# Optimization experiments

Measured on AMD Instinct MI355X. Metric: run time of the kernel, lower is better.

The kernel has to match this reference:

```python
import jax, jax.numpy as jnp
import numpy as np
from jax.scipy.special import logsumexp

B, T, D, C = 64, 512, 1024, 32


def setup_inputs() -> dict:
    key = jax.random.key(0)
    ks = jax.random.split(key, 6)
    vectors = jax.random.normal(ks[0], (B, T, D), dtype=jnp.float32)
    mask = jnp.ones((B, T), dtype=jnp.int32)
    targets = jax.random.randint(ks[1], (B, T), 0, C)
    W = jax.random.normal(ks[2], (C, D), dtype=jnp.float32) * 0.02
    b = jnp.zeros((C,), dtype=jnp.float32)
    transitions = jax.random.normal(ks[3], (C, C), dtype=jnp.float32) * 0.1
    start_transitions = jax.random.normal(ks[4], (C,), dtype=jnp.float32) * 0.1
    end_transitions = jax.random.normal(ks[5], (C,), dtype=jnp.float32) * 0.1
    return {"vectors": vectors, "mask": mask, "targets": targets, "W": W, "b": b,
            "transitions": transitions, "start_transitions": start_transitions,
            "end_transitions": end_transitions}


def reference(vectors, mask, targets, W, b, transitions, start_transitions, end_transitions):
    n_classes = transitions.shape[0]
    # projection: [B,T,C]
    logits = jnp.einsum('btd,cd->btc', vectors, W) + b
    maskf = mask.astype(logits.dtype)

    # time-major views for scan
    logits_tm = jnp.swapaxes(logits, 0, 1)   # [T,B,C]
    mask_tm = jnp.swapaxes(maskf, 0, 1)      # [T,B]

    # ---- CRF partition function (forward algorithm, log-sum-exp recurrence) ----
    def fwd_step(alpha, xs):
        lt, mt = xs                                      # [B,C], [B]
        inner = alpha[:, :, None] + transitions[None] + lt[:, None, :]  # [B,C,C]
        new = logsumexp(inner, axis=1)                   # [B,C]
        alpha = jnp.where(mt[:, None] > 0, new, alpha)
        return alpha, None

    alpha0 = start_transitions[None, :] + logits_tm[0]
    alpha, _ = jax.lax.scan(fwd_step, alpha0, (logits_tm[1:], mask_tm[1:]))
    log_Z = logsumexp(alpha + end_transitions[None, :], axis=-1)  # [B]

    # ---- joint (numerator) score of the target path, AllenNLP semantics ----
    emit = jnp.take_along_axis(logits, targets[..., None], axis=-1)[..., 0]  # [B,T]
    trans_sc = transitions[targets[:, :-1], targets[:, 1:]]                  # [B,T-1]
    score = start_transitions[targets[:, 0]]
    score = score + jnp.sum(trans_sc * maskf[:, 1:], axis=1)
    score = score + jnp.sum(emit[:, :-1] * maskf[:, :-1], axis=1)
    last_idx = jnp.sum(mask, axis=1).astype(jnp.int32) - 1                   # [B]
    last_tags = jnp.take_along_axis(targets, last_idx[:, None], axis=1)[:, 0]
    score = score + end_transitions[last_tags]
    score = score + jnp.take_along_axis(logits[:, -1], last_tags[:, None], axis=1)[:, 0] * maskf[:, -1]

    # loss = -log_likelihood / num_tokens
    loss = -jnp.sum(score - log_Z) / jnp.sum(maskf)

    # ---- Viterbi decoding (max-product DP + backtrace) ----
    def vit_step(delta, xs):
        lt, mt = xs
        inner = delta[:, :, None] + transitions[None]    # [B,C,C] (prev x next)
        bp = jnp.argmax(inner, axis=1)                   # [B,C]
        best = jnp.max(inner, axis=1) + lt
        new_delta = jnp.where(mt[:, None] > 0, best, delta)
        bp = jnp.where(mt[:, None] > 0, bp, jnp.arange(n_classes)[None, :])
        return new_delta, bp

    delta0 = start_transitions[None, :] + logits_tm[0]
    delta, bps = jax.lax.scan(vit_step, delta0, (logits_tm[1:], mask_tm[1:]))  # bps [T-1,B,C]
    final = delta + end_transitions[None, :]
    path_scores = jnp.max(final, axis=-1)                # [B]
    last_tag = jnp.argmax(final, axis=-1)                # [B]

    def back_step(tag, bp_t):
        prev = jnp.take_along_axis(bp_t, tag[:, None], axis=1)[:, 0]
        return prev, tag

    first_tag, tags_rev = jax.lax.scan(back_step, last_tag, bps, reverse=True)  # ys[t] = tag at t+1
    tags = jnp.concatenate([first_tag[:, None], jnp.swapaxes(tags_rev, 0, 1)], axis=1)  # [B,T]

    return loss, logits, tags, path_scores
```

## Files before the change

kernel.cpp:

```cpp
#include <hip/hip_runtime.h>

#define B_ 64
#define T_ 512
#define D_ 1024
#define C_ 32
#define KCH 64
#define CHUNK 16
#define NCHUNK (T_ / CHUNK)
#define NEG_INF (-1e30f)

__device__ __forceinline__ float bcast0(float v) {
  return __uint_as_float(__builtin_amdgcn_readfirstlane(__float_as_uint(v)));
}
__device__ __forceinline__ float rlane(float v, int l) {
  return __uint_as_float(__builtin_amdgcn_readlane(__float_as_uint(v), l));
}

__global__ __launch_bounds__(256) void k_logits(const float* __restrict__ vec,
                                                const float* __restrict__ W,
                                                const float* __restrict__ bias,
                                                float* __restrict__ out) {
  __shared__ __align__(16) float vt[64][KCH + 4];
  __shared__ __align__(16) float wt[32][KCH + 4];
  const int tid = threadIdx.x;
  const int cg = tid & 7;
  const int rg = tid >> 3;
  const int r0 = blockIdx.x * 64;
  const int sr = tid >> 4;
  const int sq = tid & 15;
  const int wr = tid >> 3;
  const int wq = tid & 7;
  float acc[2][4];
#pragma unroll
  for (int a = 0; a < 2; ++a)
#pragma unroll
    for (int bb = 0; bb < 4; ++bb) acc[a][bb] = 0.f;

  for (int c = 0; c < D_ / KCH; ++c) {
    const int k0 = c * KCH;
    __syncthreads();
#pragma unroll
    for (int p = 0; p < 4; ++p) {
      const int r = p * 16 + sr;
      float4 v = *(const float4*)(vec + (size_t)(r0 + r) * D_ + k0 + sq * 4);
      *(float4*)&vt[r][sq * 4] = v;
    }
    {
      float4 a = *(const float4*)(W + (size_t)wr * D_ + k0 + wq * 4);
      float4 b2 = *(const float4*)(W + (size_t)wr * D_ + k0 + (wq + 8) * 4);
      *(float4*)&wt[wr][wq * 4] = a;
      *(float4*)&wt[wr][(wq + 8) * 4] = b2;
    }
    __syncthreads();
#pragma unroll 2
    for (int k = 0; k < KCH; k += 4) {
      float4 v[2], w[4];
#pragma unroll
      for (int rr = 0; rr < 2; ++rr) v[rr] = *(const float4*)&vt[rg + rr * 32][k];
#pragma unroll
      for (int cc = 0; cc < 4; ++cc) w[cc] = *(const float4*)&wt[cg + cc * 8][k];
#pragma unroll
      for (int rr = 0; rr < 2; ++rr)
#pragma unroll
        for (int cc = 0; cc < 4; ++cc) {
          acc[rr][cc] = fmaf(v[rr].x, w[cc].x, acc[rr][cc]);
          acc[rr][cc] = fmaf(v[rr].y, w[cc].y, acc[rr][cc]);
          acc[rr][cc] = fmaf(v[rr].z, w[cc].z, acc[rr][cc]);
          acc[rr][cc] = fmaf(v[rr].w, w[cc].w, acc[rr][cc]);
        }
    }
  }
#pragma unroll
  for (int rr = 0; rr < 2; ++rr) {
    const size_t row = (size_t)(r0 + rg + rr * 32);
#pragma unroll
    for (int cc = 0; cc < 4; ++cc) {
      const int c = cg + cc * 8;
      out[row * C_ + c] = acc[rr][cc] + bias[c];
    }
  }
}

__global__ __launch_bounds__(64) void k_crf(const float* __restrict__ lg,
                                            const int* __restrict__ mask,
                                            const int* __restrict__ tgt,
                                            const float* __restrict__ trans,
                                            const float* __restrict__ st,
                                            const float* __restrict__ et,
                                            float* __restrict__ wsp,
                                            float* __restrict__ tags_out,
                                            float* __restrict__ path_out) {
  __shared__ __align__(16) float dsh[256 * C_];
  __shared__ __align__(16) float a_sh[C_];
  __shared__ __align__(16) float Lsh[2][CHUNK * C_];
  __shared__ float s0_sh[T_];
  __shared__ int mk_sh[T_];
  __shared__ unsigned char bp[(T_ - 1) * C_];
  __shared__ unsigned char tagb[T_];
  __shared__ unsigned char c8[64 * C_];
  __shared__ int btag[64];

  const int tid = threadIdx.x;
  const int b = blockIdx.x & 63;
  const int role = blockIdx.x >> 6;
  const int j = tid & 31;
  const int h = tid >> 5;
  const float* L = lg + (size_t)b * T_ * C_;
  const int* mk = mask + b * T_;

  float pre[8];
#pragma unroll
  for (int i = 0; i < 8; ++i) pre[i] = L[i * 64 + tid];
  {
    int4 m0 = *(const int4*)(mk + tid * 4);
    int4 m1 = *(const int4*)(mk + 256 + tid * 4);
    *(int4*)&mk_sh[tid * 4] = m0;
    *(int4*)&mk_sh[256 + tid * 4] = m1;
  }

  if (role == 0) {
    float ET[32];
#pragma unroll
    for (int i = 0; i < 32; ++i) ET[i] = __expf(trans[i * C_ + j]);
    const float a0j = st[j] + L[j];
    const float m0 = bcast0(a0j);
    float vp = __expf(a0j - m0);
    a_sh[j] = vp;
#pragma unroll
    for (int i = 0; i < 8; ++i) {
      const float b0v = rlane(pre[i], 0);
      const float b1v = rlane(pre[i], 32);
      const float base = (tid < 32) ? b0v : b1v;
      Lsh[0][i * 64 + tid] = __expf(pre[i] - base);
    }
    for (int c = 0; c < NCHUNK; ++c) {
      if (c < NCHUNK - 1) {
#pragma unroll
        for (int i = 0; i < 8; ++i) pre[i] = L[(c + 1) * (CHUNK * C_) + i * 64 + tid];
      }
      const float* Fs = Lsh[c & 1];
      const int tlo = c ? c * CHUNK : 1;
      const int thi = c * CHUNK + CHUNK;
      for (int t = tlo; t < thi; ++t) {
        const float Fv = Fs[(t - c * CHUNK) * C_ + j];
        const int mc = mk_sh[t];
        float4 q = *(const float4*)&a_sh[0];
        float s0 = q.x * ET[0], s1 = q.y * ET[1], s2 = q.z * ET[2], s3 = q.w * ET[3];
#pragma unroll
        for (int g = 1; g < 8; ++g) {
          q = *(const float4*)&a_sh[g * 4];
          s0 = fmaf(q.x, ET[4 * g + 0], s0);
          s1 = fmaf(q.y, ET[4 * g + 1], s1);
          s2 = fmaf(q.z, ET[4 * g + 2], s2);
          s3 = fmaf(q.w, ET[4 * g + 3], s3);
        }
        const float sv = (s0 + s1) + (s2 + s3);
        const float s0b = bcast0(sv);
        const float r = __builtin_amdgcn_rcpf(s0b);
        const float pn = sv * r * Fv;
        vp = (mc > 0) ? pn : vp;
        if (tid == 0) s0_sh[t] = (mc > 0) ? s0b : 1.0f;
        a_sh[j] = vp;
      }
      if (c < NCHUNK - 1) {
#pragma unroll
        for (int i = 0; i < 8; ++i) {
          const float b0v = rlane(pre[i], 0);
          const float b1v = rlane(pre[i], 32);
          const float base = (tid < 32) ? b0v : b1v;
          Lsh[(c & 1) ^ 1][i * 64 + tid] = __expf(pre[i] - base);
        }
      }
    }
    float lsum = 0.f, csum = 0.f;
#pragma unroll
    for (int kk = 0; kk < 8; ++kk) {
      const int t = tid + kk * 64;
      if (t >= 1) {
        lsum += __logf(s0_sh[t]);
        if (mk_sh[t] > 0) csum += L[(size_t)t * C_];
      }
    }
#pragma unroll
    for (int d = 32; d; d >>= 1) { lsum += __shfl_xor(lsum, d); csum += __shfl_xor(csum, d); }
    const float mT = m0 + lsum + csum;
    float val = (tid < 32) ? (mT + __logf(vp) + et[j]) : NEG_INF;
    float mm = val;
#pragma unroll
    for (int d = 32; d; d >>= 1) mm = fmaxf(mm, __shfl_xor(mm, d));
    float ee = __expf(val - mm);
#pragma unroll
    for (int d = 32; d; d >>= 1) ee += __shfl_xor(ee, d);
    const float logZ = mm + __logf(ee);
    float sc = 0.f, msf = 0.f;
#pragma unroll
    for (int kk = 0; kk < 8; ++kk) {
      const int t = tid + kk * 64;
      const float mf = (float)mk_sh[t];
      const int tg = tgt[b * T_ + t];
      msf += mf;
      float contrib = 0.f;
      if (t >= 1) contrib += trans[tgt[b * T_ + t - 1] * C_ + tg];
      if (t <= T_ - 2) contrib += L[t * C_ + tg];
      sc = fmaf(mf, contrib, sc);
    }
#pragma unroll
    for (int d = 32; d; d >>= 1) { sc += __shfl_xor(sc, d); msf += __shfl_xor(msf, d); }
    if (tid == 0) {
      int last_idx = (int)msf - 1;
      if (last_idx < 0) last_idx = 0;
      const int lt = tgt[b * T_ + last_idx];
      float s = sc + st[tgt[b * T_]] + et[lt];
      s = fmaf((float)mk_sh[T_ - 1], L[(T_ - 1) * C_ + lt], s);
      wsp[b] = logZ;
      wsp[64 + b] = s;
      wsp[128 + b] = msf;
    }
  } else {
    float TT[32];
#pragma unroll
    for (int i = 0; i < 32; ++i) TT[i] = trans[i * C_ + j];
#pragma unroll
    for (int i = 0; i < 8; ++i) Lsh[0][i * 64 + tid] = pre[i];
    float vdj = st[j] + L[j];
    dsh[j] = vdj;

    auto phase2 = [&](int tb) {
#pragma unroll 2
      for (int it = 0; it < 128; ++it) {
        const int t = tb + 2 * it + h;
        if (t < T_) {
          const float* dr = &dsh[((t - 1) & 255) * C_];
          float best; int idx;
          {
            float4 q = *(const float4*)&dr[28];
            best = q.w + TT[31]; idx = 31;
            float cx = q.z + TT[30]; bool ge = cx >= best; best = ge ? cx : best; idx = ge ? 30 : idx;
            cx = q.y + TT[29]; ge = cx >= best; best = ge ? cx : best; idx = ge ? 29 : idx;
            cx = q.x + TT[28]; ge = cx >= best; best = ge ? cx : best; idx = ge ? 28 : idx;
          }
#pragma unroll
          for (int g = 6; g >= 0; --g) {
            float4 q = *(const float4*)&dr[4 * g];
            float cx = q.w + TT[4 * g + 3]; bool ge = cx >= best; best = ge ? cx : best; idx = ge ? 4 * g + 3 : idx;
            cx = q.z + TT[4 * g + 2]; ge = cx >= best; best = ge ? cx : best; idx = ge ? 4 * g + 2 : idx;
            cx = q.y + TT[4 * g + 1]; ge = cx >= best; best = ge ? cx : best; idx = ge ? 4 * g + 1 : idx;
            cx = q.x + TT[4 * g + 0]; ge = cx >= best; best = ge ? cx : best; idx = ge ? 4 * g + 0 : idx;
          }
          const int bpv = (mk_sh[t] > 0) ? idx : j;
          bp[(t - 1) * C_ + j] = (unsigned char)bpv;
        }
      }
    };

    for (int c = 0; c < NCHUNK; ++c) {
      if (c < NCHUNK - 1) {
#pragma unroll
        for (int i = 0; i < 8; ++i) pre[i] = L[(c + 1) * (CHUNK * C_) + i * 64 + tid];
      }
      const float* Ls = Lsh[c & 1];
      const int tlo = c ? c * CHUNK : 1;
      const int thi = c * CHUNK + CHUNK;
      for (int t = tlo; t < thi; ++t) {
        const float lc = Ls[(t - c * CHUNK) * C_ + j];
        const int mc = mk_sh[t];
        const float* dr = &dsh[((t - 1) & 255) * C_];
        float gm[8];
#pragma unroll
        for (int g = 0; g < 8; ++g) {
          float4 q = *(const float4*)&dr[4 * g];
          const float c0 = q.x + TT[4 * g + 0];
          const float c1 = q.y + TT[4 * g + 1];
          const float c2 = q.z + TT[4 * g + 2];
          const float c3 = q.w + TT[4 * g + 3];
          gm[g] = fmaxf(fmaxf(c0, c1), fmaxf(c2, c3));
        }
        const float m01 = fmaxf(gm[0], gm[1]), m23 = fmaxf(gm[2], gm[3]);
        const float m45 = fmaxf(gm[4], gm[5]), m67 = fmaxf(gm[6], gm[7]);
        const float bestv = fmaxf(fmaxf(m01, m23), fmaxf(m45, m67));
        vdj = (mc > 0) ? (bestv + lc) : vdj;
        dsh[(t & 255) * C_ + j] = vdj;
      }
      if (c < NCHUNK - 1) {
#pragma unroll
        for (int i = 0; i < 8; ++i) Lsh[(c & 1) ^ 1][i * 64 + tid] = pre[i];
      }
      if (c == 15) phase2(1);
    }
    phase2(257);

    float fv = (tid < 32) ? (vdj + et[j]) : NEG_INF;
    int fi = (tid < 32) ? j : 64;
#pragma unroll
    for (int d = 32; d; d >>= 1) {
      const float ov = __shfl_xor(fv, d);
      const int oi = __shfl_xor(fi, d);
      if (ov > fv || (ov == fv && oi < fi)) { fv = ov; fi = oi; }
    }
    const int last_tag = fi;
    if (tid == 0) path_out[b] = fv;
    int cur[32];
#pragma unroll
    for (int e = 0; e < 32; ++e) cur[e] = (tid + 64 * e) & 31;
#pragma unroll
    for (int s = 0; s < 8; ++s) {
#pragma unroll
      for (int e = 0; e < 32; ++e) {
        const int m = (tid + 64 * e) >> 5;
        const int r = 8 * m + 7 - s;
        if (r <= T_ - 2) cur[e] = bp[r * C_ + cur[e]];
      }
    }
#pragma unroll
    for (int e = 0; e < 32; ++e) c8[tid + 64 * e] = (unsigned char)cur[e];
    if (tid == 0) {
      int c = last_tag;
      tagb[T_ - 1] = (unsigned char)c;
      for (int m = 63; m >= 0; --m) { c = c8[m * C_ + c]; btag[m] = c; }
    }
    {
      const int m = tid;
      const int rhi = (m == 63) ? (T_ - 2) : (8 * m + 7);
      int c = (m == 63) ? last_tag : btag[m + 1];
#pragma unroll
      for (int s = 0; s < 7; ++s) {
        const int r = rhi - s;
        if (r >= 8 * m + 1) { c = bp[r * C_ + c]; tagb[r] = (unsigned char)c; }
      }
      tagb[8 * m] = (unsigned char)btag[m];
    }
#pragma unroll
    for (int kk = 0; kk < 8; ++kk) {
      const int t = tid + kk * 64;
      tags_out[b * T_ + t] = (float)tagb[t];
    }
  }
}

__global__ __launch_bounds__(64) void k_loss(const float* __restrict__ wsp, float* __restrict__ out0) {
  const int tid = threadIdx.x;
  float d = wsp[64 + tid] - wsp[tid];
  float m = wsp[128 + tid];
#pragma unroll
  for (int s = 32; s; s >>= 1) { d += __shfl_xor(d, s); m += __shfl_xor(m, s); }
  if (tid == 0) out0[0] = -d / m;
}

extern "C" void kernel_launch(void* const* d_in, const int* in_sizes, int n_in,
                              void* d_out, int out_size, void* d_ws, size_t ws_size,
                              hipStream_t stream) {
  (void)in_sizes; (void)n_in; (void)out_size; (void)ws_size;
  const float* vec  = (const float*)d_in[0];
  const int* mask   = (const int*)d_in[1];
  const int* tgt    = (const int*)d_in[2];
  const float* W    = (const float*)d_in[3];
  const float* bias = (const float*)d_in[4];
  const float* tr   = (const float*)d_in[5];
  const float* st   = (const float*)d_in[6];
  const float* et   = (const float*)d_in[7];
  float* out = (float*)d_out;
  float* logits = out + 1;
  float* tags = out + 1 + (size_t)B_ * T_ * C_;
  float* path = tags + (size_t)B_ * T_;
  float* wsp = (float*)d_ws;

  hipLaunchKernelGGL(k_logits, dim3(512), dim3(256), 0, stream, vec, W, bias, logits);
  hipLaunchKernelGGL(k_crf, dim3(128), dim3(64), 0, stream, logits, mask, tgt, tr, st, et, wsp, tags, path);
  hipLaunchKernelGGL(k_loss, dim3(1), dim3(64), 0, stream, wsp, out);
}
```

Measured before the change: 428.4 us.

## Replace LDS state exchange in CRF recurrences with DPP/shuffle butterfly permutations

The forward (logsumexp) and Viterbi max recurrences no longer write the per-step state vector to LDS and read it back as float4s. Each lane now gathers all 32 predecessor values through a butterfly of one shuffle and several DPP ops, with the transition tables pre-permuted to match (MU ordering). Logits are streamed straight into registers 16 steps at a time instead of through a double-buffered LDS staging area. This aims to cut LDS round-trip latency on the serial critical path, at the cost of more cross-lane instructions and higher register pressure; the phase2 backpointer pass now reloads the unpermuted transition row.

Result: no change. 436.4 us (+1.9%).

```diff
diff --git a/kernel.cpp b/kernel.cpp
--- a/kernel.cpp
+++ b/kernel.cpp
@@ -5,16 +5,34 @@
 #define D_ 1024
 #define C_ 32
 #define KCH 64
-#define CHUNK 16
-#define NCHUNK (T_ / CHUNK)
 #define NEG_INF (-1e30f)
 
 __device__ __forceinline__ float bcast0(float v) {
   return __uint_as_float(__builtin_amdgcn_readfirstlane(__float_as_uint(v)));
 }
-__device__ __forceinline__ float rlane(float v, int l) {
-  return __uint_as_float(__builtin_amdgcn_readlane(__float_as_uint(v), l));
-}
+
+#define DPPF(x, ctrl) \
+  __uint_as_float(__builtin_amdgcn_update_dpp(0, (int)__float_as_uint(x), (ctrl), 0xF, 0xF, true))
+#define CTL_X1 0xB1
+#define CTL_X2 0x4E
+#define CTL_X7 0x141
+#define CTL_XF 0x140
+
+#define MU_INIT {0,16,1,17,2,18,3,19,7,23,6,22,5,21,4,20, \
+                 15,31,14,30,13,29,12,28,8,24,9,25,10,26,11,27}
+
+#define BFLY(x, val)                                                    \
+  {                                                                     \
+    val[0] = (x);                                                       \
+    val[1] = __shfl_xor((x), 16);                                       \
+    val[2] = DPPF(val[0], CTL_X1);  val[3] = DPPF(val[1], CTL_X1);      \
+    _Pragma("unroll")                                                   \
+    for (int k_ = 0; k_ < 4; ++k_) val[4 + k_] = DPPF(val[k_], CTL_X2); \
+    _Pragma("unroll")                                                   \
+    for (int k_ = 0; k_ < 8; ++k_) val[8 + k_] = DPPF(val[k_], CTL_X7); \
+    _Pragma("unroll")                                                   \
+    for (int k_ = 0; k_ < 16; ++k_) val[16 + k_] = DPPF(val[k_], CTL_XF); \
+  }
 
 __global__ __launch_bounds__(256) void k_logits(const float* __restrict__ vec,
                                                 const float* __restrict__ W,
@@ -91,8 +109,6 @@
                                             float* __restrict__ tags_out,
                                             float* __restrict__ path_out) {
   __shared__ __align__(16) float dsh[256 * C_];
-  __shared__ __align__(16) float a_sh[C_];
-  __shared__ __align__(16) float Lsh[2][CHUNK * C_];
   __shared__ float s0_sh[T_];
   __shared__ int mk_sh[T_];
   __shared__ unsigned char bp[(T_ - 1) * C_];
@@ -108,9 +124,6 @@
   const float* L = lg + (size_t)b * T_ * C_;
   const int* mk = mask + b * T_;
 
-  float pre[8];
-#pragma unroll
-  for (int i = 0; i < 8; ++i) pre[i] = L[i * 64 + tid];
   {
     int4 m0 = *(const int4*)(mk + tid * 4);
     int4 m1 = *(const int4*)(mk + 256 + tid * 4);
@@ -118,58 +131,56 @@
     *(int4*)&mk_sh[256 + tid * 4] = m1;
   }
 
+  constexpr int MU[32] = MU_INIT;
+
+  float Lc[16], Ln[16];
+#pragma unroll
+  for (int i = 0; i < 16; ++i) Lc[i] = L[i * C_ + j];
+
   if (role == 0) {
-    float ET[32];
-#pragma unroll
-    for (int i = 0; i < 32; ++i) ET[i] = __expf(trans[i * C_ + j]);
-    const float a0j = st[j] + L[j];
+    float ET2[32];
+#pragma unroll
+    for (int r = 0; r < 32; ++r) ET2[r] = __expf(trans[(j ^ MU[r]) * C_ + j]);
+    float Fc[16];
+#pragma unroll
+    for (int i = 0; i < 16; ++i) Fc[i] = __expf(Lc[i] - bcast0(Lc[i]));
+    const float a0j = st[j] + Lc[0];
     const float m0 = bcast0(a0j);
     float vp = __expf(a0j - m0);
-    a_sh[j] = vp;
-#pragma unroll
-    for (int i = 0; i < 8; ++i) {
-      const float b0v = rlane(pre[i], 0);
-      const float b1v = rlane(pre[i], 32);
-      const float base = (tid < 32) ? b0v : b1v;
-      Lsh[0][i * 64 + tid] = __expf(pre[i] - base);
-    }
-    for (int c = 0; c < NCHUNK; ++c) {
-      if (c < NCHUNK - 1) {
-#pragma unroll
-        for (int i = 0; i < 8; ++i) pre[i] = L[(c + 1) * (CHUNK * C_) + i * 64 + tid];
-      }
-      const float* Fs = Lsh[c & 1];
-      const int tlo = c ? c * CHUNK : 1;
-      const int thi = c * CHUNK + CHUNK;
-      for (int t = tlo; t < thi; ++t) {
-        const float Fv = Fs[(t - c * CHUNK) * C_ + j];
-        const int mc = mk_sh[t];
-        float4 q = *(const float4*)&a_sh[0];
-        float s0 = q.x * ET[0], s1 = q.y * ET[1], s2 = q.z * ET[2], s3 = q.w * ET[3];
+    for (int c = 0; c < 32; ++c) {
+      int Mc[16];
+#pragma unroll
+      for (int i = 0; i < 16; ++i) Mc[i] = mk_sh[c * 16 + i];
+      if (c < 31) {
+#pragma unroll
+        for (int i = 0; i < 16; ++i) Ln[i] = L[((c + 1) * 16 + i) * C_ + j];
+      }
+#pragma unroll
+      for (int i = 0; i < 16; ++i) {
+        if (i == 0 && c == 0) continue;
+        const int t = c * 16 + i;
+        const int mc = Mc[i];
+        float val[32];
+        BFLY(vp, val);
+        float s0 = val[0] * ET2[0], s1 = val[1] * ET2[1];
+        float s2 = val[2] * ET2[2], s3 = val[3] * ET2[3];
 #pragma unroll
         for (int g = 1; g < 8; ++g) {
-          q = *(const float4*)&a_sh[g * 4];
-          s0 = fmaf(q.x, ET[4 * g + 0], s0);
-          s1 = fmaf(q.y, ET[4 * g + 1], s1);
-          s2 = fmaf(q.z, ET[4 * g + 2], s2);
-          s3 = fmaf(q.w, ET[4 * g + 3], s3);
+          s0 = fmaf(val[4 * g + 0], ET2[4 * g + 0], s0);
+          s1 = fmaf(val[4 * g + 1], ET2[4 * g + 1], s1);
+          s2 = fmaf(val[4 * g + 2], ET2[4 * g + 2], s2);
+          s3 = fmaf(val[4 * g + 3], ET2[4 * g + 3], s3);
         }
         const float sv = (s0 + s1) + (s2 + s3);
         const float s0b = bcast0(sv);
         const float r = __builtin_amdgcn_rcpf(s0b);
-        const float pn = sv * r * Fv;
+        const float pn = sv * r * Fc[i];
         vp = (mc > 0) ? pn : vp;
         if (tid == 0) s0_sh[t] = (mc > 0) ? s0b : 1.0f;
-        a_sh[j] = vp;
-      }
-      if (c < NCHUNK - 1) {
-#pragma unroll
-        for (int i = 0; i < 8; ++i) {
-          const float b0v = rlane(pre[i], 0);
-          const float b1v = rlane(pre[i], 32);
-          const float base = (tid < 32) ? b0v : b1v;
-          Lsh[(c & 1) ^ 1][i * 64 + tid] = __expf(pre[i] - base);
-        }
+      }
+      if (c < 31) {
+#pragma unroll
+        for (int i = 0; i < 16; ++i) { Lc[i] = Ln[i]; Fc[i] = __expf(Lc[i] - bcast0(Lc[i])); }
       }
     }
     float lsum = 0.f, csum = 0.f;
@@ -184,11 +195,11 @@
 #pragma unroll
     for (int d = 32; d; d >>= 1) { lsum += __shfl_xor(lsum, d); csum += __shfl_xor(csum, d); }
     const float mT = m0 + lsum + csum;
-    float val = (tid < 32) ? (mT + __logf(vp) + et[j]) : NEG_INF;
-    float mm = val;
+    float val_ = (tid < 32) ? (mT + __logf(vp) + et[j]) : NEG_INF;
+    float mm = val_;
 #pragma unroll
     for (int d = 32; d; d >>= 1) mm = fmaxf(mm, __shfl_xor(mm, d));
-    float ee = __expf(val - mm);
+    float ee = __expf(val_ - mm);
 #pragma unroll
     for (int d = 32; d; d >>= 1) ee += __shfl_xor(ee, d);
     const float logZ = mm + __logf(ee);
@@ -217,15 +228,16 @@
       wsp[128 + b] = msf;
     }
   } else {
-    float TT[32];
-#pragma unroll
-    for (int i = 0; i < 32; ++i) TT[i] = trans[i * C_ + j];
-#pragma unroll
-    for (int i = 0; i < 8; ++i) Lsh[0][i * 64 + tid] = pre[i];
-    float vdj = st[j] + L[j];
-    dsh[j] = vdj;
+    float TT2[32];
+#pragma unroll
+    for (int r = 0; r < 32; ++r) TT2[r] = trans[(j ^ MU[r]) * C_ + j];
+    float vdj = st[j] + Lc[0];
+    dsh[(size_t)0 * C_ + j] = vdj;
 
     auto phase2 = [&](int tb) {
+      float TTo[32];
+#pragma unroll
+      for (int i = 0; i < 32; ++i) TTo[i] = trans[i * C_ + j];
 #pragma unroll 2
       for (int it = 0; it < 128; ++it) {
         const int t = tb + 2 * it + h;
@@ -234,18 +246,18 @@
           float best; int idx;
           {
             float4 q = *(const float4*)&dr[28];
-            best = q.w + TT[31]; idx = 31;
-            float cx = q.z + TT[30]; bool ge = cx >= best; best = ge ? cx : best; idx = ge ? 30 : idx;
-            cx = q.y + TT[29]; ge = cx >= best; best = ge ? cx : best; idx = ge ? 29 : idx;
-            cx = q.x + TT[28]; ge = cx >= best; best = ge ? cx : best; idx = ge ? 28 : idx;
+            best = q.w + TTo[31]; idx = 31;
+            float cx = q.z + TTo[30]; bool ge = cx >= best; best = ge ? cx : best; idx = ge ? 30 : idx;
+            cx = q.y + TTo[29]; ge = cx >= best; best = ge ? cx : best; idx = ge ? 29 : idx;
+            cx = q.x + TTo[28]; ge = cx >= best; best = ge ? cx : best; idx = ge ? 28 : idx;
           }
 #pragma unroll
           for (int g = 6; g >= 0; --g) {
             float4 q = *(const float4*)&dr[4 * g];
-            float cx = q.w + TT[4 * g + 3]; bool ge = cx >= best; best = ge ? cx : best; idx = ge ? 4 * g + 3 : idx;
-            cx = q.z + TT[4 * g + 2]; ge = cx >= best; best = ge ? cx : best; idx = ge ? 4 * g + 2 : idx;
-            cx = q.y + TT[4 * g + 1]; ge = cx >= best; best = ge ? cx : best; idx = ge ? 4 * g + 1 : idx;
-            cx = q.x + TT[4 * g + 0]; ge = cx >= best; best = ge ? cx : best; idx = ge ? 4 * g + 0 : idx;
+            float cx = q.w + TTo[4 * g + 3]; bool ge = cx >= best; best = ge ? cx : best; idx = ge ? 4 * g + 3 : idx;
+            cx = q.z + TTo[4 * g + 2]; ge = cx >= best; best = ge ? cx : best; idx = ge ? 4 * g + 2 : idx;
+            cx = q.y + TTo[4 * g + 1]; ge = cx >= best; best = ge ? cx : best; idx = ge ? 4 * g + 1 : idx;
+            cx = q.x + TTo[4 * g + 0]; ge = cx >= best; best = ge ? cx : best; idx = ge ? 4 * g + 0 : idx;
           }
           const int bpv = (mk_sh[t] > 0) ? idx : j;
           bp[(t - 1) * C_ + j] = (unsigned char)bpv;
@@ -253,37 +265,45 @@
       }
     };
 
-    for (int c = 0; c < NCHUNK; ++c) {
-      if (c < NCHUNK - 1) {
-#pragma unroll
-        for (int i = 0; i < 8; ++i) pre[i] = L[(c + 1) * (CHUNK * C_) + i * 64 + tid];
-      }
-      const float* Ls = Lsh[c & 1];
-      const int tlo = c ? c * CHUNK : 1;
-      const int thi = c * CHUNK + CHUNK;
-      for (int t = tlo; t < thi; ++t) {
-        const float lc = Ls[(t - c * CHUNK) * C_ + j];
-        const int mc = mk_sh[t];
-        const float* dr = &dsh[((t - 1) & 255) * C_];
-        float gm[8];
-#pragma unroll
-        for (int g = 0; g < 8; ++g) {
-          float4 q = *(const float4*)&dr[4 * g];
-          const float c0 = q.x + TT[4 * g + 0];
-          const float c1 = q.y + TT[4 * g + 1];
-          const float c2 = q.z + TT[4 * g + 2];
-          const float c3 = q.w + TT[4 * g + 3];
-          gm[g] = fmaxf(fmaxf(c0, c1), fmaxf(c2, c3));
-        }
-        const float m01 = fmaxf(gm[0], gm[1]), m23 = fmaxf(gm[2], gm[3]);
-        const float m45 = fmaxf(gm[4], gm[5]), m67 = fmaxf(gm[6], gm[7]);
-        const float bestv = fmaxf(fmaxf(m01, m23), fmaxf(m45, m67));
-        vdj = (mc > 0) ? (bestv + lc) : vdj;
+    for (int c = 0; c < 32; ++c) {
+      int Mc[16];
+#pragma unroll
+      for (int i = 0; i < 16; ++i) Mc[i] = mk_sh[c * 16 + i];
+      if (c < 31) {
+#pragma unroll
+        for (int i = 0; i < 16; ++i) Ln[i] = L[((c + 1) * 16 + i) * C_ + j];
+      }
+#pragma unroll
+      for (int i = 0; i < 16; ++i) {
+        if (i == 0 && c == 0) continue;
+        const int t = c * 16 + i;
+        const int mc = Mc[i];
+        float val[32];
+        BFLY(vdj, val);
+        float gm0 = fmaxf(fmaxf(val[0] + TT2[0], val[1] + TT2[1]),
+                          fmaxf(val[2] + TT2[2], val[3] + TT2[3]));
+        float gm1 = fmaxf(fmaxf(val[4] + TT2[4], val[5] + TT2[5]),
+                          fmaxf(val[6] + TT2[6], val[7] + TT2[7]));
+        float gm2 = fmaxf(fmaxf(val[8] + TT2[8], val[9] + TT2[9]),
+                          fmaxf(val[10] + TT2[10], val[11] + TT2[11]));
+        float gm3 = fmaxf(fmaxf(val[12] + TT2[12], val[13] + TT2[13]),
+                          fmaxf(val[14] + TT2[14], val[15] + TT2[15]));
+        float gm4 = fmaxf(fmaxf(val[16] + TT2[16], val[17] + TT2[17]),
+                          fmaxf(val[18] + TT2[18], val[19] + TT2[19]));
+        float gm5 = fmaxf(fmaxf(val[20] + TT2[20], val[21] + TT2[21]),
+                          fmaxf(val[22] + TT2[22], val[23] + TT2[23]));
+        float gm6 = fmaxf(fmaxf(val[24] + TT2[24], val[25] + TT2[25]),
+                          fmaxf(val[26] + TT2[26], val[27] + TT2[27]));
+        float gm7 = fmaxf(fmaxf(val[28] + TT2[28], val[29] + TT2[29]),
+                          fmaxf(val[30] + TT2[30], val[31] + TT2[31]));
+        const float bestv = fmaxf(fmaxf(fmaxf(gm0, gm1), fmaxf(gm2, gm3)),
+                                  fmaxf(fmaxf(gm4, gm5), fmaxf(gm6, gm7)));
+        vdj = (mc > 0) ? (bestv + Lc[i]) : vdj;
         dsh[(t & 255) * C_ + j] = vdj;
       }
-      if (c < NCHUNK - 1) {
-#pragma unroll
-        for (int i = 0; i < 8; ++i) Lsh[(c & 1) ^ 1][i * 64 + tid] = pre[i];
+      if (c < 31) {
+#pragma unroll
+        for (int i = 0; i < 16; ++i) Lc[i] = Ln[i];
       }
       if (c == 15) phase2(1);
     }
```
